# Kernel tuning notes

Measured on AMD Instinct MI355X. Metric: run time of the kernel, lower is better.

The kernel has to match this reference:

```python
import jax, jax.numpy as jnp
import numpy as np
from jax import lax

BETA = 0.3

def setup_inputs() -> dict:
    key = jax.random.key(0)
    ks = jax.random.split(key, 5)
    B, C, H, W = 1, 64, 96, 96
    x = jax.random.normal(ks[0], (B, C, H, W), dtype=jnp.float32)
    # d_conv: Conv2d(C, C, k=3, stride=1, padding=2, dilation=2)
    dW = jax.random.normal(ks[1], (C, C, 3, 3), dtype=jnp.float32) * 0.05
    db = jax.random.normal(ks[2], (C,), dtype=jnp.float32) * 0.05
    # conv: Conv2d(C, C, k=1)
    cW = jax.random.normal(ks[3], (C, C, 1, 1), dtype=jnp.float32) * 0.1
    cb = jax.random.normal(ks[4], (C,), dtype=jnp.float32) * 0.05
    return {"x": x, "dW": dW, "db": db, "cW": cW, "cb": cb}

def _conv(x, w, b, padding, dilation):
    y = lax.conv_general_dilated(
        x, w, window_strides=(1, 1),
        padding=[(padding, padding), (padding, padding)],
        rhs_dilation=(dilation, dilation),
        dimension_numbers=("NCHW", "OIHW", "NCHW"))
    return y + b[None, :, None, None]

def reference(x, dW, db, cW, cb):
    B, C, H, W = x.shape
    HW = H * W
    y = _conv(x, dW, db, padding=2, dilation=2)   # (B,C,H,W), same d_conv used for q and k
    v = _conv(x, cW, cb, padding=0, dilation=1).reshape(B, HW, C)
    # NOTE: torch uses raw .reshape (not transpose) for q — faithful here.
    q = y.reshape(B, HW, C)
    k = y.reshape(B, C, HW)
    qk = jnp.einsum("bnc,bcm->bnm", q, k)         # (B,HW,HW)
    qk = jnp.where(jnp.abs(qk) > BETA, qk, 0.0)   # threshold mask (qk*mask)
    att = jax.nn.softmax(qk, axis=-1)
    att = jnp.einsum("bnm,bmc->bnc", att, v)      # (B,HW,C)
    att = att.swapaxes(1, 2).reshape(B, C, H, W)
    return x + att
```

## Files before the change

### kernel.cpp

```cpp
#include <hip/hip_runtime.h>
#include <hip/hip_bf16.h>

#define CC 64
#define HW 9216
#define IMG 96
#define SPLITS 16
#define SPLEN 576
#define ITERS 9
#define LOG2E 1.44269504f
#define RESC 5.545f

typedef _Float16 f16;
typedef __attribute__((ext_vector_type(8))) _Float16 f16x8;
typedef __attribute__((ext_vector_type(4))) _Float16 f16x4;
typedef __attribute__((ext_vector_type(4))) float f32x4;
typedef __attribute__((ext_vector_type(16))) float f32x16;
typedef __attribute__((ext_vector_type(4))) unsigned int u32x4;

__global__ __launch_bounds__(256) void prepad_kernel(
    const float* __restrict__ x, const float* __restrict__ dW, const float* __restrict__ cW,
    f16* __restrict__ xt, f16* __restrict__ dWt, f16* __restrict__ cWt)
{
    __shared__ float tile[32][65];
    const int t = threadIdx.x;
    if (blockIdx.x >= 313) {
        const int wb = blockIdx.x - 313;
        #pragma unroll
        for (int j = 0; j < 4; ++j) {
            int idx = wb * 1024 + j * 256 + t;
            if (idx < 36864) {
                float val = dW[idx];
                int co = idx / 576;
                int r = idx - co * 576;
                int ci = r / 9, tap = r - ci * 9;
                dWt[tap * 4096 + co * 64 + ci] = (f16)val;
            } else {
                int c = idx - 36864;
                cWt[c] = (f16)cW[c];
            }
        }
        return;
    }
    const int p0 = blockIdx.x * 32;
    const int pl = t & 31;
    const int p = p0 + pl;
    int r = p / 100, c = p % 100;
    bool interior = (r >= 2) && (r < 98) && (c >= 2) && (c < 98);
    int img = (r - 2) * IMG + (c - 2);
    #pragma unroll
    for (int j = 0; j < 8; ++j) {
        int ci = j * 8 + (t >> 5);
        tile[pl][ci] = interior ? x[ci * HW + img] : 0.f;
    }
    __syncthreads();
    const int row16 = t >> 4, chunk = t & 15;
    #pragma unroll
    for (int j = 0; j < 2; ++j) {
        int row = j * 16 + row16;
        int pr = p0 + row;
        if (pr < 10000) {
            f16x4 hv = {(f16)tile[row][chunk * 4 + 0], (f16)tile[row][chunk * 4 + 1],
                        (f16)tile[row][chunk * 4 + 2], (f16)tile[row][chunk * 4 + 3]};
            *(f16x4*)&xt[pr * 64 + chunk * 4] = hv;
        }
    }
}

__global__ __launch_bounds__(64) void conv_mfma_kernel(
    const f16* __restrict__ xt, const f16* __restrict__ dWt, const float* __restrict__ db,
    const f16* __restrict__ cWt, const float* __restrict__ cb,
    f16* __restrict__ yq, f16* __restrict__ kt, f16* __restrict__ vt)
{
    const int b = blockIdx.x;
    const int tile = b >> 2, cog = b & 3;
    const int co0 = cog * 16;
    const int L = threadIdx.x;
    const int g = L >> 4, c16 = L & 15;

    f16x8 Bf[9][2], Bv[2];
    #pragma unroll
    for (int tap = 0; tap < 9; ++tap)
        #pragma unroll
        for (int kc = 0; kc < 2; ++kc)
            Bf[tap][kc] = *(const f16x8*)&dWt[(tap * 64 + co0 + c16) * 64 + g * 8 + kc * 32];
    #pragma unroll
    for (int kc = 0; kc < 2; ++kc)
        Bv[kc] = *(const f16x8*)&cWt[(co0 + c16) * 64 + g * 8 + kc * 32];

    const int ms = tile * 16;
    const int h = ms / IMG, wc = ms % IMG;
    const int pb = (h + 2) * 100 + (wc + 2) + c16;

    f32x4 accY = (f32x4){0.f, 0.f, 0.f, 0.f};
    f32x4 accV = (f32x4){0.f, 0.f, 0.f, 0.f};

    #pragma unroll
    for (int tap = 0; tap < 9; ++tap) {
        int kh = tap / 3, kw = tap % 3;
        int toff = (2 * kh - 2) * 100 + (2 * kw - 2);
        const f16* ap = xt + (pb + toff) * 64;
        f16x8 A0 = *(const f16x8*)(ap + g * 8);
        f16x8 A1 = *(const f16x8*)(ap + g * 8 + 32);
        accY = __builtin_amdgcn_mfma_f32_16x16x32_f16(A0, Bf[tap][0], accY, 0, 0, 0);
        accY = __builtin_amdgcn_mfma_f32_16x16x32_f16(A1, Bf[tap][1], accY, 0, 0, 0);
        if (tap == 4) {
            accV = __builtin_amdgcn_mfma_f32_16x16x32_f16(A0, Bv[0], accV, 0, 0, 0);
            accV = __builtin_amdgcn_mfma_f32_16x16x32_f16(A1, Bv[1], accV, 0, 0, 0);
        }
    }

    const float dbv = db[co0 + c16], cbv = cb[co0 + c16];
    f16 hy[4];
    #pragma unroll
    for (int j = 0; j < 4; ++j) hy[j] = (f16)(accY[j] + dbv);
    *(f16x4*)&yq[(co0 + c16) * HW + ms + 4 * g] = (f16x4){hy[0], hy[1], hy[2], hy[3]};
    #pragma unroll
    for (int j = 0; j < 4; ++j)
        kt[(ms + 4 * g + j) * 64 + co0 + c16] = hy[j];
    #pragma unroll
    for (int j = 0; j < 4; ++j) {
        int m = ms + 4 * g + j;
        vt[(m & 63) * HW + (co0 + c16) * 144 + (m >> 6)] = (f16)(accV[j] + cbv);
    }
}

__global__ __launch_bounds__(256, 4) void attn_kernel(
    const f16* __restrict__ kt, const f16* __restrict__ vt, const f16* __restrict__ yq,
    f16* __restrict__ acc_ws, float* __restrict__ m_ws, float* __restrict__ l_ws)
{
    __shared__ f16 sKT[64 * 64];
    __shared__ f16 sVT[64 * 64];
    __shared__ float sAL[4 * 32];

    const int t = threadIdx.x;
    const int L = t & 63, w = t >> 6;
    const int l5 = L >> 5, l31 = L & 31;
    const int x7 = l31 & 7;
    const int qb = blockIdx.x >> 4, sp = blockIdx.x & (SPLITS - 1);
    const int n0 = qb * 128;
    const int mbase = sp * SPLEN;
    float* alw = (float*)sAL + w * 32;

    const int srow0 = t >> 3, sch = t & 7;
    const int srow1 = srow0 + 32;
    const int dst0 = srow0 * 64 + ((sch ^ (srow0 & 7)) << 3);
    const int dst1 = srow1 * 64 + ((sch ^ (srow1 & 7)) << 3);

    f16x8 qf[4];
    #pragma unroll
    for (int kc = 0; kc < 4; ++kc)
        qf[kc] = *(const f16x8*)(yq + (n0 + w * 32 + l31) * 64 + kc * 16 + l5 * 8);

    float mi = -1e30f, mtrue = -1e30f, li = 0.f;
    f32x16 acc[2];
    #pragma unroll
    for (int ct = 0; ct < 2; ++ct)
        #pragma unroll
        for (int r = 0; r < 16; ++r) acc[ct][r] = 0.f;

    for (int it = 0; it < ITERS; ++it) {
        const int m0 = mbase + it * 64;
        __syncthreads();
        *(uint4*)&sKT[dst0] = *(const uint4*)&kt[(m0 + srow0) * 64 + sch * 8];
        *(uint4*)&sKT[dst1] = *(const uint4*)&kt[(m0 + srow1) * 64 + sch * 8];
        *(uint4*)&sVT[dst0] = *(const uint4*)&vt[srow0 * HW + m0 + sch * 8];
        *(uint4*)&sVT[dst1] = *(const uint4*)&vt[srow1 * HW + m0 + sch * 8];
        __syncthreads();

        f32x16 st[2];
        #pragma unroll
        for (int kt2 = 0; kt2 < 2; ++kt2) {
            f32x16 d;
            #pragma unroll
            for (int r = 0; r < 16; ++r) d[r] = 0.f;
            #pragma unroll
            for (int kc = 0; kc < 4; ++kc) {
                f16x8 af = *(const f16x8*)&sKT[(kt2 * 32 + l31) * 64 + ((((kc << 1) | l5) ^ x7) << 3)];
                d = __builtin_amdgcn_mfma_f32_32x32x16_f16(af, qf[kc], d, 0, 0, 0);
            }
            st[kt2] = d;
        }
        #pragma unroll
        for (int kt2 = 0; kt2 < 2; ++kt2)
            #pragma unroll
            for (int r = 0; r < 16; ++r)
                st[kt2][r] = (fabsf(st[kt2][r]) > 0.3f) ? st[kt2][r] : 0.f;

        float q8[8];
        #pragma unroll
        for (int kt2 = 0; kt2 < 2; ++kt2)
            #pragma unroll
            for (int rq = 0; rq < 4; ++rq)
                q8[kt2 * 4 + rq] = fmaxf(fmaxf(st[kt2][rq * 4 + 0], st[kt2][rq * 4 + 1]),
                                         fmaxf(st[kt2][rq * 4 + 2], st[kt2][rq * 4 + 3]));
        float mx = fmaxf(fmaxf(fmaxf(q8[0], q8[1]), fmaxf(q8[2], q8[3])),
                         fmaxf(fmaxf(q8[4], q8[5]), fmaxf(q8[6], q8[7])));
        mx = fmaxf(mx, __shfl_xor(mx, 32, 64));
        mtrue = fmaxf(mtrue, mx);

        unsigned long long need = __ballot(mx > mi + RESC);
        float mnew = need ? fmaxf(mi, mx) : mi;
        float nL = mnew * LOG2E;
        float alpha = __builtin_amdgcn_exp2f(mi * LOG2E - nL);

        float ls = 0.f;
        unsigned int u[2][4][2];
        #pragma unroll
        for (int kt2 = 0; kt2 < 2; ++kt2)
            #pragma unroll
            for (int rq = 0; rq < 4; ++rq) {
                float p0 = __builtin_amdgcn_exp2f(fmaf(st[kt2][rq * 4 + 0], LOG2E, -nL));
                float p1 = __builtin_amdgcn_exp2f(fmaf(st[kt2][rq * 4 + 1], LOG2E, -nL));
                float p2 = __builtin_amdgcn_exp2f(fmaf(st[kt2][rq * 4 + 2], LOG2E, -nL));
                float p3 = __builtin_amdgcn_exp2f(fmaf(st[kt2][rq * 4 + 3], LOG2E, -nL));
                ls += (p0 + p1) + (p2 + p3);
                u[kt2][rq][0] = __builtin_bit_cast(unsigned int, __builtin_amdgcn_cvt_pkrtz(p0, p1));
                u[kt2][rq][1] = __builtin_bit_cast(unsigned int, __builtin_amdgcn_cvt_pkrtz(p2, p3));
            }

        if (need) {
            li = li * alpha + ls;
            if (l5 == 0) alw[l31] = alpha;
            f32x4 aj[4];
            #pragma unroll
            for (int rq = 0; rq < 4; ++rq)
                aj[rq] = *(const f32x4*)&alw[rq * 8 + l5 * 4];
            #pragma unroll
            for (int ct = 0; ct < 2; ++ct)
                #pragma unroll
                for (int r = 0; r < 16; ++r)
                    acc[ct][r] *= aj[r >> 2][r & 3];
        } else {
            li += ls;
        }
        mi = mnew;

        #pragma unroll
        for (int kc = 0; kc < 4; ++kc) {
            const int kt2 = kc >> 1;
            const int rq0 = (kc & 1) * 2, rq1 = rq0 + 1;
            auto rA = __builtin_amdgcn_permlane32_swap(
                (int)u[kt2][rq0][0], (int)u[kt2][rq1][0], false, false);
            auto rB = __builtin_amdgcn_permlane32_swap(
                (int)u[kt2][rq0][1], (int)u[kt2][rq1][1], false, false);
            u32x4 pw = {(unsigned int)rA[0], (unsigned int)rB[0],
                        (unsigned int)rA[1], (unsigned int)rB[1]};
            f16x8 pa = __builtin_bit_cast(f16x8, pw);
            #pragma unroll
            for (int ct = 0; ct < 2; ++ct) {
                int vrow = ct * 32 + l31;
                f16x8 vb = *(const f16x8*)&sVT[vrow * 64 + ((((kc << 1) | l5) ^ x7) << 3)];
                acc[ct] = __builtin_amdgcn_mfma_f32_32x32x16_f16(pa, vb, acc[ct], 0, 0, 0);
            }
        }
    }

    float fsc = __builtin_amdgcn_exp2f((mi - mtrue) * LOG2E);
    li *= fsc;
    float li_tot = li + __shfl_xor(li, 32, 64);
    if (l5 == 0) alw[l31] = fsc;
    f32x4 fj[4];
    #pragma unroll
    for (int rq = 0; rq < 4; ++rq)
        fj[rq] = *(const f32x4*)&alw[rq * 8 + l5 * 4];
    #pragma unroll
    for (int ct = 0; ct < 2; ++ct)
        #pragma unroll
        for (int r = 0; r < 16; ++r)
            acc[ct][r] *= fj[r >> 2][r & 3];

    const int base = blockIdx.x;
    #pragma unroll
    for (int ct = 0; ct < 2; ++ct)
        #pragma unroll
        for (int r = 0; r < 16; ++r) {
            int ql = w * 32 + (r & 3) + 8 * (r >> 2) + 4 * l5;
            int c  = ct * 32 + l31;
            acc_ws[base * 8192 + ql * 64 + c] = (f16)acc[ct][r];
        }
    if (l5 == 0) {
        m_ws[base * 128 + w * 32 + l31] = mtrue;
        l_ws[base * 128 + w * 32 + l31] = li_tot;
    }
}

__global__ __launch_bounds__(256) void merge_kernel(
    const f16* __restrict__ acc_ws, const float* __restrict__ m_ws, const float* __restrict__ l_ws,
    const float* __restrict__ x, float* __restrict__ out)
{
    __shared__ float wsh[SPLITS * 16];
    __shared__ float att[64 * 17];
    const int b = blockIdx.x;
    const int row0 = b * 16;
    const int qb = row0 >> 7;
    const int ql0 = row0 & 127;
    const int t = threadIdx.x;
    if (t < 16) {
        int ql = ql0 + t;
        float ms = -1e30f;
        float mv[SPLITS];
        #pragma unroll
        for (int sp = 0; sp < SPLITS; ++sp) {
            mv[sp] = m_ws[(qb * SPLITS + sp) * 128 + ql];
            ms = fmaxf(ms, mv[sp]);
        }
        float Lsum = 0.f, ev[SPLITS];
        #pragma unroll
        for (int sp = 0; sp < SPLITS; ++sp) {
            ev[sp] = __builtin_amdgcn_exp2f((mv[sp] - ms) * LOG2E);
            Lsum += l_ws[(qb * SPLITS + sp) * 128 + ql] * ev[sp];
        }
        float inv = 1.f / Lsum;
        #pragma unroll
        for (int sp = 0; sp < SPLITS; ++sp)
            wsh[sp * 16 + t] = ev[sp] * inv;
    }
    __syncthreads();
    {
        const int rr = t >> 4, c0 = (t & 15) * 4;
        float v0 = 0.f, v1 = 0.f, v2 = 0.f, v3 = 0.f;
        #pragma unroll
        for (int sp = 0; sp < SPLITS; ++sp) {
            f16x4 hv = *(const f16x4*)&acc_ws[(qb * SPLITS + sp) * 8192 + (ql0 + rr) * 64 + c0];
            float wv = wsh[sp * 16 + rr];
            v0 += (float)hv[0] * wv;
            v1 += (float)hv[1] * wv;
            v2 += (float)hv[2] * wv;
            v3 += (float)hv[3] * wv;
        }
        att[(c0 + 0) * 17 + rr] = v0;
        att[(c0 + 1) * 17 + rr] = v1;
        att[(c0 + 2) * 17 + rr] = v2;
        att[(c0 + 3) * 17 + rr] = v3;
    }
    __syncthreads();
    {
        const int c = t >> 2, r0 = (t & 3) * 4;
        const int idx = c * HW + row0 + r0;
        float4 xv = *(const float4*)&x[idx];
        float4 ov;
        ov.x = xv.x + att[c * 17 + r0 + 0];
        ov.y = xv.y + att[c * 17 + r0 + 1];
        ov.z = xv.z + att[c * 17 + r0 + 2];
        ov.w = xv.w + att[c * 17 + r0 + 3];
        *(float4*)&out[idx] = ov;
    }
}

extern "C" void kernel_launch(void* const* d_in, const int* in_sizes, int n_in,
                              void* d_out, int out_size, void* d_ws, size_t ws_size,
                              hipStream_t stream)
{
    const float* x  = (const float*)d_in[0];
    const float* dW = (const float*)d_in[1];
    const float* db = (const float*)d_in[2];
    const float* cW = (const float*)d_in[3];
    const float* cb = (const float*)d_in[4];
    float* out = (float*)d_out;

    char* ws = (char*)d_ws;
    f16* kt     = (f16*)(ws);
    f16* yq     = (f16*)(ws + 1179648);
    f16* vt     = (f16*)(ws + 2359296);
    f16* xt     = (f16*)(ws + 3538944);
    f16* dWt    = (f16*)(ws + 4818944);
    f16* cWt    = (f16*)(ws + 4892672);
    f16* acc_ws = (f16*)(ws + 4900864);
    float* m_ws = (float*)(ws + 23775232);
    float* l_ws = (float*)(ws + 24365056);

    prepad_kernel<<<dim3(353), dim3(256), 0, stream>>>(x, dW, cW, xt, dWt, cWt);
    conv_mfma_kernel<<<dim3(2304), dim3(64), 0, stream>>>(xt, dWt, db, cWt, cb, yq, kt, vt);
    attn_kernel<<<dim3(72 * SPLITS), dim3(256), 0, stream>>>(kt, vt, yq, acc_ws, m_ws, l_ws);
    merge_kernel<<<dim3(576), dim3(256), 0, stream>>>(acc_ws, m_ws, l_ws, x, out);
}
```

Baseline: 131.6 us.

## Fuse split-K merge into attention kernel via last-block atomic counter

Removes the separate merge kernel launch. Each attention block bumps a per-query-block atomic counter after writing its partial results, and the last of the 16 split blocks does the log-sum-exp merge and the residual add for all 128 rows. The counters are zeroed in the conv kernel. This saves one launch and its tail, but the merge now runs on only 72 blocks, serialised at the end of each group. It also adds about 13KB of shared memory to the attention kernel, which may lower occupancy.

```diff
diff --git a/kernel.cpp b/kernel.cpp
--- a/kernel.cpp
+++ b/kernel.cpp
@@ -69,13 +69,18 @@
 __global__ __launch_bounds__(64) void conv_mfma_kernel(
     const f16* __restrict__ xt, const f16* __restrict__ dWt, const float* __restrict__ db,
     const f16* __restrict__ cWt, const float* __restrict__ cb,
-    f16* __restrict__ yq, f16* __restrict__ kt, f16* __restrict__ vt)
+    f16* __restrict__ yq, f16* __restrict__ kt, f16* __restrict__ vt,
+    int* __restrict__ cnt)
 {
     const int b = blockIdx.x;
     const int tile = b >> 2, cog = b & 3;
     const int co0 = cog * 16;
     const int L = threadIdx.x;
     const int g = L >> 4, c16 = L & 15;
+
+    if (b == 0) {
+        for (int i = L; i < 72; i += 64) cnt[i] = 0;
+    }
 
     f16x8 Bf[9][2], Bv[2];
     #pragma unroll
@@ -126,11 +131,15 @@
 
 __global__ __launch_bounds__(256, 4) void attn_kernel(
     const f16* __restrict__ kt, const f16* __restrict__ vt, const f16* __restrict__ yq,
-    f16* __restrict__ acc_ws, float* __restrict__ m_ws, float* __restrict__ l_ws)
+    f16* __restrict__ acc_ws, float* __restrict__ m_ws, float* __restrict__ l_ws,
+    int* __restrict__ cnt, const float* __restrict__ x, float* __restrict__ out)
 {
     __shared__ f16 sKT[64 * 64];
     __shared__ f16 sVT[64 * 64];
     __shared__ float sAL[4 * 32];
+    __shared__ float wshL[SPLITS * 128];
+    __shared__ float attL[64 * 17];
+    __shared__ int sLast;
 
     const int t = threadIdx.x;
     const int L = t & 63, w = t >> 6;
@@ -282,68 +291,67 @@
         m_ws[base * 128 + w * 32 + l31] = mtrue;
         l_ws[base * 128 + w * 32 + l31] = li_tot;
     }
-}
-
-__global__ __launch_bounds__(256) void merge_kernel(
-    const f16* __restrict__ acc_ws, const float* __restrict__ m_ws, const float* __restrict__ l_ws,
-    const float* __restrict__ x, float* __restrict__ out)
-{
-    __shared__ float wsh[SPLITS * 16];
-    __shared__ float att[64 * 17];
-    const int b = blockIdx.x;
-    const int row0 = b * 16;
-    const int qb = row0 >> 7;
-    const int ql0 = row0 & 127;
-    const int t = threadIdx.x;
-    if (t < 16) {
-        int ql = ql0 + t;
-        float ms = -1e30f;
+
+    __threadfence();
+    if (t == 0) {
+        int old = atomicAdd(&cnt[qb], 1);
+        sLast = (old == SPLITS - 1) ? 1 : 0;
+    }
+    __syncthreads();
+    if (!sLast) return;
+    __threadfence();
+
+    if (t < 128) {
+        const int ql = t;
+        float msx = -1e30f;
         float mv[SPLITS];
         #pragma unroll
-        for (int sp = 0; sp < SPLITS; ++sp) {
-            mv[sp] = m_ws[(qb * SPLITS + sp) * 128 + ql];
-            ms = fmaxf(ms, mv[sp]);
-        }
-        float Lsum = 0.f, ev[SPLITS];
-        #pragma unroll
-        for (int sp = 0; sp < SPLITS; ++sp) {
-            ev[sp] = __builtin_amdgcn_exp2f((mv[sp] - ms) * LOG2E);
-            Lsum += l_ws[(qb * SPLITS + sp) * 128 + ql] * ev[sp];
+        for (int s2 = 0; s2 < SPLITS; ++s2) {
+            mv[s2] = m_ws[(qb * SPLITS + s2) * 128 + ql];
+            msx = fmaxf(msx, mv[s2]);
+        }
+        float Lsum = 0.f;
+        #pragma unroll
+        for (int s2 = 0; s2 < SPLITS; ++s2) {
+            float e = __builtin_amdgcn_exp2f((mv[s2] - msx) * LOG2E);
+            Lsum += l_ws[(qb * SPLITS + s2) * 128 + ql] * e;
+            wshL[s2 * 128 + ql] = e;
         }
         float inv = 1.f / Lsum;
         #pragma unroll
-        for (int sp = 0; sp < SPLITS; ++sp)
-            wsh[sp * 16 + t] = ev[sp] * inv;
+        for (int s2 = 0; s2 < SPLITS; ++s2)
+            wshL[s2 * 128 + ql] *= inv;
     }
     __syncthreads();
-    {
+
+    for (int ch = 0; ch < 8; ++ch) {
         const int rr = t >> 4, c0 = (t & 15) * 4;
+        const int qlr = ch * 16 + rr;
         float v0 = 0.f, v1 = 0.f, v2 = 0.f, v3 = 0.f;
         #pragma unroll
-        for (int sp = 0; sp < SPLITS; ++sp) {
-            f16x4 hv = *(const f16x4*)&acc_ws[(qb * SPLITS + sp) * 8192 + (ql0 + rr) * 64 + c0];
-            float wv = wsh[sp * 16 + rr];
+        for (int s2 = 0; s2 < SPLITS; ++s2) {
+            f16x4 hv = *(const f16x4*)&acc_ws[(qb * SPLITS + s2) * 8192 + qlr * 64 + c0];
+            float wv = wshL[s2 * 128 + qlr];
             v0 += (float)hv[0] * wv;
             v1 += (float)hv[1] * wv;
             v2 += (float)hv[2] * wv;
             v3 += (float)hv[3] * wv;
         }
-        att[(c0 + 0) * 17 + rr] = v0;
-        att[(c0 + 1) * 17 + rr] = v1;
-        att[(c0 + 2) * 17 + rr] = v2;
-        att[(c0 + 3) * 17 + rr] = v3;
-    }
-    __syncthreads();
-    {
+        attL[(c0 + 0) * 17 + rr] = v0;
+        attL[(c0 + 1) * 17 + rr] = v1;
+        attL[(c0 + 2) * 17 + rr] = v2;
+        attL[(c0 + 3) * 17 + rr] = v3;
+        __syncthreads();
         const int c = t >> 2, r0 = (t & 3) * 4;
-        const int idx = c * HW + row0 + r0;
+        const int idx = c * HW + n0 + ch * 16 + r0;
         float4 xv = *(const float4*)&x[idx];
         float4 ov;
-        ov.x = xv.x + att[c * 17 + r0 + 0];
-        ov.y = xv.y + att[c * 17 + r0 + 1];
-        ov.z = xv.z + att[c * 17 + r0 + 2];
-        ov.w = xv.w + att[c * 17 + r0 + 3];
+        ov.x = xv.x + attL[c * 17 + r0 + 0];
+        ov.y = xv.y + attL[c * 17 + r0 + 1];
+        ov.z = xv.z + attL[c * 17 + r0 + 2];
+        ov.w = xv.w + attL[c * 17 + r0 + 3];
         *(float4*)&out[idx] = ov;
+        __syncthreads();
     }
 }
 
@@ -368,9 +376,10 @@
     f16* acc_ws = (f16*)(ws + 4900864);
     float* m_ws = (float*)(ws + 23775232);
     float* l_ws = (float*)(ws + 24365056);
+    int*   cnt  = (int*)(ws + 24954880);
 
     prepad_kernel<<<dim3(353), dim3(256), 0, stream>>>(x, dW, cW, xt, dWt, cWt);
-    conv_mfma_kernel<<<dim3(2304), dim3(64), 0, stream>>>(xt, dWt, db, cWt, cb, yq, kt, vt);
-    attn_kernel<<<dim3(72 * SPLITS), dim3(256), 0, stream>>>(kt, vt, yq, acc_ws, m_ws, l_ws);
-    merge_kernel<<<dim3(576), dim3(256), 0, stream>>>(acc_ws, m_ws, l_ws, x, out);
+    conv_mfma_kernel<<<dim3(2304), dim3(64), 0, stream>>>(xt, dWt, db, cWt, cb, yq, kt, vt, cnt);
+    attn_kernel<<<dim3(72 * SPLITS), dim3(256), 0, stream>>>(kt, vt, yq, acc_ws, m_ws, l_ws,
+                                                             cnt, x, out);
 }
```

Measured after the change: 296.3 us. 2.25x slower.
